# Kernel tuning notes

Measured on AMD Instinct MI355X. Metric: run time of the kernel, lower is better.

## Reference

```python
import jax, jax.numpy as jnp
import numpy as np

NEG_SLOPE = 0.2  # PyG GATConv default


def gat_layer(x, src, dst, W, a_src, a_dst, b, num_nodes):
    """Single-head GATConv (heads=1, add_self_loops handled by caller)."""
    xw = x @ W  # [N, H]
    s_src = xw @ a_src  # [N] per-node source attention logits
    s_dst = xw @ a_dst  # [N]
    e = jax.nn.leaky_relu(s_src[src] + s_dst[dst], NEG_SLOPE)  # [E]
    # segment softmax over incoming edges of each dst node
    m = jax.ops.segment_max(e, dst, num_segments=num_nodes)  # [N]
    ex = jnp.exp(e - m[dst])
    denom = jax.ops.segment_sum(ex, dst, num_segments=num_nodes)  # [N]
    alpha = ex / denom[dst]  # [E]
    out = jax.ops.segment_sum(alpha[:, None] * xw[src], dst, num_segments=num_nodes)
    return out + b


def setup_inputs() -> dict:
    key = jax.random.key(0)
    N, F_IN, H, E, B = 100000, 256, 64, 1000000, 16384
    ks = jax.random.split(key, 16)
    s = lambda fan: 1.0 / np.sqrt(fan)
    return {
        "x": jax.random.normal(ks[0], (N, F_IN), dtype=jnp.float32),
        "edge_index": jax.random.randint(ks[1], (2, E), 0, N, dtype=jnp.int64),
        "user_indices": jax.random.randint(ks[2], (B,), 0, N, dtype=jnp.int64),
        "movie_indices": jax.random.randint(ks[3], (B,), 0, N, dtype=jnp.int64),
        "W1": jax.random.normal(ks[4], (F_IN, H), dtype=jnp.float32) * s(F_IN),
        "a_src1": jax.random.normal(ks[5], (H,), dtype=jnp.float32) * s(H),
        "a_dst1": jax.random.normal(ks[6], (H,), dtype=jnp.float32) * s(H),
        "b1": jnp.zeros((H,), dtype=jnp.float32),
        "W2": jax.random.normal(ks[7], (H, H), dtype=jnp.float32) * s(H),
        "a_src2": jax.random.normal(ks[8], (H,), dtype=jnp.float32) * s(H),
        "a_dst2": jax.random.normal(ks[9], (H,), dtype=jnp.float32) * s(H),
        "b2": jnp.zeros((H,), dtype=jnp.float32),
        "fc_W": jax.random.normal(ks[10], (2 * H, 1), dtype=jnp.float32) * s(2 * H),
        "fc_b": jnp.zeros((1,), dtype=jnp.float32),
    }


def reference(x, edge_index, user_indices, movie_indices,
              W1, a_src1, a_dst1, b1, W2, a_src2, a_dst2, b2, fc_W, fc_b):
    N = x.shape[0]
    # PyG GATConv default add_self_loops=True: append (i, i) edges
    loops = jnp.arange(N, dtype=edge_index.dtype)
    src = jnp.concatenate([edge_index[0], loops])
    dst = jnp.concatenate([edge_index[1], loops])
    h = gat_layer(x, src, dst, W1, a_src1, a_dst1, b1, N)
    h = jax.nn.relu(h)
    h = gat_layer(h, src, dst, W2, a_src2, a_dst2, b2, N)
    combined = jnp.concatenate([h[user_indices], h[movie_indices]], axis=1)  # [B, 2H]
    return combined @ fc_W + fc_b  # [B, 1]
```

## Files before the change

### kernel.cpp

```cpp
#include <hip/hip_runtime.h>
#include <hip/hip_bf16.h>
#include <hip/hip_fp16.h>

#define LRELU_SLOPE 0.2f

__device__ __forceinline__ float lrelu(float x) { return x > 0.f ? x : LRELU_SLOPE * x; }

typedef __attribute__((ext_vector_type(8))) short short8;
typedef __attribute__((ext_vector_type(4))) float f32x4;

__device__ __forceinline__ unsigned short f2bf(float f) {
    unsigned u = __builtin_bit_cast(unsigned, f);
    u = (u + 0x7FFFu + ((u >> 16) & 1u)) >> 16;
    return (unsigned short)u;
}
__device__ __forceinline__ float bf2f(unsigned short b) {
    unsigned u = ((unsigned)b) << 16;
    return __builtin_bit_cast(float, u);
}

template <int K>
__device__ __forceinline__ void packW_body(const float* __restrict__ W,
                                           unsigned short* __restrict__ Bhi,
                                           unsigned short* __restrict__ Blo,
                                           int blk, int t) {
    constexpr int NKC = K / 32;
    int g = blk * 256 + t;
    if (g >= 4 * NKC * 64) return;
    int lane = g & 63;
    int kc = (g >> 6) % NKC;
    int ct = g / (64 * NKC);
    int qd = lane >> 4, col = lane & 15;
    #pragma unroll
    for (int j = 0; j < 8; j++) {
        int k = kc * 32 + qd * 8 + j;
        float w = W[(size_t)k * 64 + ct * 16 + col];
        unsigned short h = f2bf(w);
        float rem = w - bf2f(h);
        Bhi[(size_t)g * 8 + j] = h;
        Blo[(size_t)g * 8 + j] = f2bf(rem);
    }
}

__global__ __launch_bounds__(256) void k_prep(const float* __restrict__ W1,
                                              unsigned short* __restrict__ b1hi, unsigned short* __restrict__ b1lo,
                                              const float* __restrict__ W2,
                                              unsigned short* __restrict__ b2hi, unsigned short* __restrict__ b2lo,
                                              int* __restrict__ deg, int* __restrict__ gcnt, int N) {
    int b = blockIdx.x;
    if (b < 8)  { packW_body<256>(W1, b1hi, b1lo, b, threadIdx.x); return; }
    if (b < 10) { packW_body<64>(W2, b2hi, b2lo, b - 8, threadIdx.x); return; }
    int i = (b - 10) * 256 + threadIdx.x;
    if (i < N) deg[i] = 0;
    if (i == 0) *gcnt = 0;
}

__global__ void k_hist(const int* __restrict__ dst, int* __restrict__ deg,
                       int* __restrict__ epos, int E) {
    int i = blockIdx.x * blockDim.x + threadIdx.x;
    if (i < E) epos[i] = atomicAdd(&deg[dst[i]], 1);
}

__global__ __launch_bounds__(256) void k_offsets(const int* __restrict__ deg, int* __restrict__ start,
                                                 int2* __restrict__ sd2, int* __restrict__ gcnt, int N) {
    int idx = blockIdx.x * 256 + threadIdx.x;
    int lane = threadIdx.x & 63;
    int v = (idx < N) ? deg[idx] : 0;
    int incl = v;
    #pragma unroll
    for (int d = 1; d < 64; d <<= 1) {
        int u = __shfl_up(incl, d);
        if (lane >= d) incl += u;
    }
    int total = __shfl(incl, 63);
    int base = 0;
    if (lane == 0) base = atomicAdd(gcnt, total);
    base = __shfl(base, 0);
    int st = base + incl - v;
    if (idx < N) {
        start[idx] = st;
        sd2[idx] = make_int2(st, v);
    }
}

__global__ void k_scatter(const int* __restrict__ src, const int* __restrict__ dst,
                          const int* __restrict__ start, const int* __restrict__ epos,
                          int* __restrict__ csr, int E) {
    int i = blockIdx.x * blockDim.x + threadIdx.x;
    if (i < E) csr[start[dst[i]] + epos[i]] = src[i];
}

template <int K>
__global__ __launch_bounds__(256) void k_mfma(const float* __restrict__ X,
                                              const unsigned short* __restrict__ Bhi,
                                              const unsigned short* __restrict__ Blo,
                                              const float* __restrict__ a_s, const float* __restrict__ a_d,
                                              __half* __restrict__ XW, float* __restrict__ Ssrc,
                                              float* __restrict__ Sdst, int N) {
    constexpr int NKC = K / 32;
    int t = threadIdx.x, lane = t & 63, wid = t >> 6;
    int mtile = blockIdx.x * 4 + wid;
    if (mtile * 16 >= N) return;
    int m0 = mtile * 16;
    int qd = lane >> 4, col = lane & 15;

    int rA = m0 + col;
    rA = rA < N ? rA : N - 1;
    const float* xrow = X + (size_t)rA * K + qd * 8;

    const short8* bh = (const short8*)Bhi;
    const short8* bl = (const short8*)Blo;

    f32x4 acc[4];
    #pragma unroll
    for (int ct = 0; ct < 4; ct++) acc[ct] = (f32x4){0.f, 0.f, 0.f, 0.f};

    #pragma clang loop unroll(disable)
    for (int kc = 0; kc < NKC; kc++) {
        const float* xp = xrow + kc * 32;
        float4 xa = *(const float4*)xp;
        float4 xb = *(const float4*)(xp + 4);
        float xv[8] = {xa.x, xa.y, xa.z, xa.w, xb.x, xb.y, xb.z, xb.w};
        short8 ah, al;
        #pragma unroll
        for (int j = 0; j < 8; j++) {
            unsigned short h = f2bf(xv[j]);
            ah[j] = (short)h;
            al[j] = (short)f2bf(xv[j] - bf2f(h));
        }
        #pragma unroll
        for (int ct = 0; ct < 4; ct++) {
            short8 wh = bh[(ct * NKC + kc) * 64 + lane];
            short8 wl = bl[(ct * NKC + kc) * 64 + lane];
            acc[ct] = __builtin_amdgcn_mfma_f32_16x16x32_bf16(ah, wh, acc[ct], 0, 0, 0);
            acc[ct] = __builtin_amdgcn_mfma_f32_16x16x32_bf16(al, wh, acc[ct], 0, 0, 0);
            acc[ct] = __builtin_amdgcn_mfma_f32_16x16x32_bf16(ah, wl, acc[ct], 0, 0, 0);
        }
    }

    float asx[4], adx[4];
    #pragma unroll
    for (int ct = 0; ct < 4; ct++) {
        asx[ct] = a_s[ct * 16 + col];
        adx[ct] = a_d[ct * 16 + col];
    }
    #pragma unroll
    for (int r = 0; r < 4; r++) {
        int row = m0 + qd * 4 + r;
        if (row < N) {
            float vs = 0.f, vd = 0.f;
            #pragma unroll
            for (int ct = 0; ct < 4; ct++) {
                float v = acc[ct][r];
                XW[(size_t)row * 64 + ct * 16 + col] = __float2half(v);
                vs += v * asx[ct];
                vd += v * adx[ct];
            }
            #pragma unroll
            for (int d = 1; d < 16; d <<= 1) {
                vs += __shfl_xor(vs, d);
                vd += __shfl_xor(vd, d);
            }
            if (col == 0) { Ssrc[row] = vs; Sdst[row] = vd; }
        }
    }
}

__global__ __launch_bounds__(256) void k_attn(const __half* __restrict__ XW, const float* __restrict__ Ssrc,
                                              const float* __restrict__ Sdst, const int* __restrict__ csr,
                                              const int2* __restrict__ sd2,
                                              const float* __restrict__ bias, float* __restrict__ H,
                                              int N, int do_relu) {
    int t = threadIdx.x, lane = t & 63, wid = t >> 6;
    int q = lane >> 4;
    int c = lane & 15;
    int n = (blockIdx.x * 4 + wid) * 4 + q;
    bool valid = n < N;
    int nc = valid ? n : N - 1;

    int2 sv = sd2[nc];
    int st = sv.x, d = sv.y;
    float sd = Sdst[nc];
    int dcap = d < 16 ? d : 16;

    int myS = 0;
    if (c < d) myS = csr[st + c];

    int s0 = __shfl(myS, q * 16 + 0), s1 = __shfl(myS, q * 16 + 1);
    int s2 = __shfl(myS, q * 16 + 2), s3 = __shfl(myS, q * 16 + 3);
    float2 rs = *(const float2*)(XW + (size_t)nc * 64 + c * 4);
    float2 r0 = *(const float2*)(XW + (size_t)s0 * 64 + c * 4);
    float2 r1 = *(const float2*)(XW + (size_t)s1 * 64 + c * 4);
    float2 r2 = *(const float2*)(XW + (size_t)s2 * 64 + c * 4);
    float2 r3 = *(const float2*)(XW + (size_t)s3 * 64 + c * 4);

    float wself = __expf(lrelu(Ssrc[nc] + sd));
    float myW = 0.f;
    if (c < d) myW = __expf(lrelu(Ssrc[myS] + sd));
    float dpart = myW + ((c == 0) ? wself : 0.f);

    float4 acc4 = make_float4(0.f, 0.f, 0.f, 0.f);
    auto accum = [&](float2 raw, float w) {
        const __half2* hp = (const __half2*)&raw;
        float2 f0 = __half22float2(hp[0]);
        float2 f1 = __half22float2(hp[1]);
        acc4.x += w * f0.x; acc4.y += w * f0.y; acc4.z += w * f1.x; acc4.w += w * f1.y;
    };

    float w0 = __shfl(myW, q * 16 + 0), w1 = __shfl(myW, q * 16 + 1);
    float w2 = __shfl(myW, q * 16 + 2), w3 = __shfl(myW, q * 16 + 3);
    accum(rs, wself);
    accum(r0, w0); accum(r1, w1); accum(r2, w2); accum(r3, w3);

    for (int i = 4; i < dcap; i += 4) {
        int t0 = __shfl(myS, q * 16 + i + 0), t1 = __shfl(myS, q * 16 + i + 1);
        int t2 = __shfl(myS, q * 16 + i + 2), t3 = __shfl(myS, q * 16 + i + 3);
        float2 q0 = *(const float2*)(XW + (size_t)t0 * 64 + c * 4);
        float2 q1 = *(const float2*)(XW + (size_t)t1 * 64 + c * 4);
        float2 q2 = *(const float2*)(XW + (size_t)t2 * 64 + c * 4);
        float2 q3 = *(const float2*)(XW + (size_t)t3 * 64 + c * 4);
        float v0 = __shfl(myW, q * 16 + i + 0), v1 = __shfl(myW, q * 16 + i + 1);
        float v2 = __shfl(myW, q * 16 + i + 2), v3 = __shfl(myW, q * 16 + i + 3);
        accum(q0, v0); accum(q1, v1); accum(q2, v2); accum(q3, v3);
    }

    for (int i = 16; i < d; i++) {
        int s = csr[st + i];
        float w = __expf(lrelu(Ssrc[s] + sd));
        if (c == 0) dpart += w;
        float2 qv = *(const float2*)(XW + (size_t)s * 64 + c * 4);
        accum(qv, w);
    }

    #pragma unroll
    for (int dd = 8; dd > 0; dd >>= 1) dpart += __shfl_xor(dpart, dd);

    if (valid) {
        float4 b4 = *(const float4*)&bias[c * 4];
        float inv = 1.f / dpart;
        float4 o;
        o.x = acc4.x * inv + b4.x;
        o.y = acc4.y * inv + b4.y;
        o.z = acc4.z * inv + b4.z;
        o.w = acc4.w * inv + b4.w;
        if (do_relu) {
            o.x = fmaxf(o.x, 0.f); o.y = fmaxf(o.y, 0.f);
            o.z = fmaxf(o.z, 0.f); o.w = fmaxf(o.w, 0.f);
        }
        *(float4*)&H[(size_t)n * 64 + c * 4] = o;
    }
}

__global__ __launch_bounds__(256) void k_head(const float* __restrict__ H, const int* __restrict__ ui,
                                              const int* __restrict__ mi, const float* __restrict__ fcW,
                                              const float* __restrict__ fcb, float* __restrict__ out, int B) {
    int t = threadIdx.x, lane = t & 63, wid = t >> 6;
    int i = blockIdx.x * 4 + wid;
    if (i >= B) return;
    int u = ui[i], m = mi[i];
    float v = H[(size_t)u * 64 + lane] * fcW[lane] + H[(size_t)m * 64 + lane] * fcW[64 + lane];
    #pragma unroll
    for (int dd = 32; dd > 0; dd >>= 1) v += __shfl_xor(v, dd);
    if (lane == 0) out[i] = v + fcb[0];
}

extern "C" void kernel_launch(void* const* d_in, const int* in_sizes, int n_in,
                              void* d_out, int out_size, void* d_ws, size_t ws_size,
                              hipStream_t stream) {
    const float* x   = (const float*)d_in[0];
    const int*   ei  = (const int*)d_in[1];
    const int*   ui  = (const int*)d_in[2];
    const int*   mi  = (const int*)d_in[3];
    const float* W1  = (const float*)d_in[4];
    const float* as1 = (const float*)d_in[5];
    const float* ad1 = (const float*)d_in[6];
    const float* b1  = (const float*)d_in[7];
    const float* W2  = (const float*)d_in[8];
    const float* as2 = (const float*)d_in[9];
    const float* ad2 = (const float*)d_in[10];
    const float* b2  = (const float*)d_in[11];
    const float* fcW = (const float*)d_in[12];
    const float* fcb = (const float*)d_in[13];
    float* out = (float*)d_out;

    const int Hdim = in_sizes[5];
    const int FIN  = in_sizes[4] / Hdim;
    const int N    = in_sizes[0] / FIN;
    const int E    = in_sizes[1] / 2;
    const int B    = in_sizes[2];

    char* w = (char*)d_ws;
    auto alloc = [&](size_t bytes) -> void* {
        void* p = (void*)w;
        w += (bytes + 255) & ~(size_t)255;
        return p;
    };
    __half* xw  = (__half*)alloc((size_t)N * 64 * 2);
    float* hbuf = (float*)alloc((size_t)N * 64 * 4);
    float* ssrc = (float*)alloc((size_t)N * 4);
    float* sdst = (float*)alloc((size_t)N * 4);
    int* deg    = (int*)alloc((size_t)N * 4);
    int* startv = (int*)alloc((size_t)N * 4);
    int2* sd2   = (int2*)alloc((size_t)N * 8);
    int* gcnt   = (int*)alloc(256);
    int* csr    = (int*)alloc((size_t)E * 4);
    int* epos   = (int*)alloc((size_t)E * 4);
    unsigned short* b1hi = (unsigned short*)alloc((size_t)4 * 8 * 64 * 8 * 2);
    unsigned short* b1lo = (unsigned short*)alloc((size_t)4 * 8 * 64 * 8 * 2);
    unsigned short* b2hi = (unsigned short*)alloc((size_t)4 * 2 * 64 * 8 * 2);
    unsigned short* b2lo = (unsigned short*)alloc((size_t)4 * 2 * 64 * 8 * 2);

    const int* esrc = ei;
    const int* edst = ei + E;

    int prepBlocks = 10 + (N + 255) / 256;
    k_prep<<<prepBlocks, 256, 0, stream>>>(W1, b1hi, b1lo, W2, b2hi, b2lo, deg, gcnt, N);

    k_hist<<<(E + 255) / 256, 256, 0, stream>>>(edst, deg, epos, E);
    k_offsets<<<(N + 255) / 256, 256, 0, stream>>>(deg, startv, sd2, gcnt, N);
    k_scatter<<<(E + 255) / 256, 256, 0, stream>>>(esrc, edst, startv, epos, csr, E);

    const int mfmaBlocks = ((N + 15) / 16 + 3) / 4;
    const int attnBlocks = (N + 15) / 16;

    k_mfma<256><<<mfmaBlocks, 256, 0, stream>>>(x, b1hi, b1lo, as1, ad1, xw, ssrc, sdst, N);
    k_attn<<<attnBlocks, 256, 0, stream>>>(xw, ssrc, sdst, csr, sd2, b1, hbuf, N, 1);

    k_mfma<64><<<mfmaBlocks, 256, 0, stream>>>(hbuf, b2hi, b2lo, as2, ad2, xw, ssrc, sdst, N);
    k_attn<<<attnBlocks, 256, 0, stream>>>(xw, ssrc, sdst, csr, sd2, b2, hbuf, N, 0);

    k_head<<<(B + 3) / 4, 256, 0, stream>>>(hbuf, ui, mi, fcW, fcb, out, B);
}
```

Baseline: 350.0 us.

## Overlap layer-1 GEMM with CSR histogram and scatter via fused launches

The layer-1 projection GEMM is split in two halves, and each half runs in extra blocks of the histogram and scatter kernels. This lets the compute-bound MFMA work share the GPU with the atomic- and scatter-bound CSR build, and it removes one launch. The risk is that the fused kernels carry the GEMM's register pressure into the simple blocks, which can lower occupancy for the atomic and scatter work.

```diff
diff --git a/kernel.cpp b/kernel.cpp
--- a/kernel.cpp
+++ b/kernel.cpp
@@ -55,12 +55,6 @@
     if (i == 0) *gcnt = 0;
 }
 
-__global__ void k_hist(const int* __restrict__ dst, int* __restrict__ deg,
-                       int* __restrict__ epos, int E) {
-    int i = blockIdx.x * blockDim.x + threadIdx.x;
-    if (i < E) epos[i] = atomicAdd(&deg[dst[i]], 1);
-}
-
 __global__ __launch_bounds__(256) void k_offsets(const int* __restrict__ deg, int* __restrict__ start,
                                                  int2* __restrict__ sd2, int* __restrict__ gcnt, int N) {
     int idx = blockIdx.x * 256 + threadIdx.x;
@@ -83,23 +77,16 @@
     }
 }
 
-__global__ void k_scatter(const int* __restrict__ src, const int* __restrict__ dst,
-                          const int* __restrict__ start, const int* __restrict__ epos,
-                          int* __restrict__ csr, int E) {
-    int i = blockIdx.x * blockDim.x + threadIdx.x;
-    if (i < E) csr[start[dst[i]] + epos[i]] = src[i];
-}
-
 template <int K>
-__global__ __launch_bounds__(256) void k_mfma(const float* __restrict__ X,
-                                              const unsigned short* __restrict__ Bhi,
-                                              const unsigned short* __restrict__ Blo,
-                                              const float* __restrict__ a_s, const float* __restrict__ a_d,
-                                              __half* __restrict__ XW, float* __restrict__ Ssrc,
-                                              float* __restrict__ Sdst, int N) {
+__device__ __forceinline__ void mfma_body(const float* __restrict__ X,
+                                          const unsigned short* __restrict__ Bhi,
+                                          const unsigned short* __restrict__ Blo,
+                                          const float* __restrict__ a_s, const float* __restrict__ a_d,
+                                          __half* __restrict__ XW, float* __restrict__ Ssrc,
+                                          float* __restrict__ Sdst, int N, int blk) {
     constexpr int NKC = K / 32;
     int t = threadIdx.x, lane = t & 63, wid = t >> 6;
-    int mtile = blockIdx.x * 4 + wid;
+    int mtile = blk * 4 + wid;
     if (mtile * 16 >= N) return;
     int m0 = mtile * 16;
     int qd = lane >> 4, col = lane & 15;
@@ -166,6 +153,51 @@
     }
 }
 
+__global__ __launch_bounds__(256) void k_hist_mfma(const int* __restrict__ dst, int* __restrict__ deg,
+                                                   int* __restrict__ epos, int E, int histBlocks,
+                                                   const float* __restrict__ X,
+                                                   const unsigned short* __restrict__ Bhi,
+                                                   const unsigned short* __restrict__ Blo,
+                                                   const float* __restrict__ a_s, const float* __restrict__ a_d,
+                                                   __half* __restrict__ XW, float* __restrict__ Ssrc,
+                                                   float* __restrict__ Sdst, int N, int mfmaBase) {
+    int b = blockIdx.x;
+    if (b < histBlocks) {
+        int i = b * 256 + threadIdx.x;
+        if (i < E) epos[i] = atomicAdd(&deg[dst[i]], 1);
+        return;
+    }
+    mfma_body<256>(X, Bhi, Blo, a_s, a_d, XW, Ssrc, Sdst, N, mfmaBase + (b - histBlocks));
+}
+
+__global__ __launch_bounds__(256) void k_scatter_mfma(const int* __restrict__ src, const int* __restrict__ dst,
+                                                      const int* __restrict__ start, const int* __restrict__ epos,
+                                                      int* __restrict__ csr, int E, int scatBlocks,
+                                                      const float* __restrict__ X,
+                                                      const unsigned short* __restrict__ Bhi,
+                                                      const unsigned short* __restrict__ Blo,
+                                                      const float* __restrict__ a_s, const float* __restrict__ a_d,
+                                                      __half* __restrict__ XW, float* __restrict__ Ssrc,
+                                                      float* __restrict__ Sdst, int N, int mfmaBase) {
+    int b = blockIdx.x;
+    if (b < scatBlocks) {
+        int i = b * 256 + threadIdx.x;
+        if (i < E) csr[start[dst[i]] + epos[i]] = src[i];
+        return;
+    }
+    mfma_body<256>(X, Bhi, Blo, a_s, a_d, XW, Ssrc, Sdst, N, mfmaBase + (b - scatBlocks));
+}
+
+template <int K>
+__global__ __launch_bounds__(256) void k_mfma(const float* __restrict__ X,
+                                              const unsigned short* __restrict__ Bhi,
+                                              const unsigned short* __restrict__ Blo,
+                                              const float* __restrict__ a_s, const float* __restrict__ a_d,
+                                              __half* __restrict__ XW, float* __restrict__ Ssrc,
+                                              float* __restrict__ Sdst, int N) {
+    mfma_body<K>(X, Bhi, Blo, a_s, a_d, XW, Ssrc, Sdst, N, blockIdx.x);
+}
+
 __global__ __launch_bounds__(256) void k_attn(const __half* __restrict__ XW, const float* __restrict__ Ssrc,
                                               const float* __restrict__ Sdst, const int* __restrict__ csr,
                                               const int2* __restrict__ sd2,
@@ -313,17 +345,21 @@
     const int* esrc = ei;
     const int* edst = ei + E;
 
+    const int mfmaBlocks = ((N + 15) / 16 + 3) / 4;
+    const int mfmaA = mfmaBlocks / 2;
+    const int mfmaB = mfmaBlocks - mfmaA;
+    const int histBlocks = (E + 255) / 256;
+    const int attnBlocks = (N + 15) / 16;
+
     int prepBlocks = 10 + (N + 255) / 256;
     k_prep<<<prepBlocks, 256, 0, stream>>>(W1, b1hi, b1lo, W2, b2hi, b2lo, deg, gcnt, N);
 
-    k_hist<<<(E + 255) / 256, 256, 0, stream>>>(edst, deg, epos, E);
+    k_hist_mfma<<<histBlocks + mfmaA, 256, 0, stream>>>(edst, deg, epos, E, histBlocks,
+                                                        x, b1hi, b1lo, as1, ad1, xw, ssrc, sdst, N, 0);
     k_offsets<<<(N + 255) / 256, 256, 0, stream>>>(deg, startv, sd2, gcnt, N);
-    k_scatter<<<(E + 255) / 256, 256, 0, stream>>>(esrc, edst, startv, epos, csr, E);
-
-    const int mfmaBlocks = ((N + 15) / 16 + 3) / 4;
-    const int attnBlocks = (N + 15) / 16;
-
-    k_mfma<256><<<mfmaBlocks, 256, 0, stream>>>(x, b1hi, b1lo, as1, ad1, xw, ssrc, sdst, N);
+    k_scatter_mfma<<<histBlocks + mfmaB, 256, 0, stream>>>(esrc, edst, startv, epos, csr, E, histBlocks,
+                                                           x, b1hi, b1lo, as1, ad1, xw, ssrc, sdst, N, mfmaA);
+
     k_attn<<<attnBlocks, 256, 0, stream>>>(xw, ssrc, sdst, csr, sd2, b1, hbuf, N, 1);
 
     k_mfma<64><<<mfmaBlocks, 256, 0, stream>>>(hbuf, b2hi, b2lo, as2, ad2, xw, ssrc, sdst, N);
```

Measured after the change: 357.4 us. 1.02x slower.

## Replace exact CSR build with fixed-stride padded adjacency plus overflow list

Applied to the files above, without the earlier changes.

Replaces the three-kernel CSR construction (histogram, prefix-sum offsets, scatter) with a single kernel that places each edge in a fixed 32-slot row per destination node. Edges beyond the 32nd go to a global overflow list, which every attention thread scans linearly. This removes two kernel launches and the epos/start passes, at the cost of a padded adjacency buffer. It also relies on degrees rarely exceeding 32, which holds for the random test graph (mean degree about 10). A large overflow list would make attention quadratic, and the overflow buffer has a fixed capacity of 65536 with no bounds check.

```diff
diff --git a/kernel.cpp b/kernel.cpp
--- a/kernel.cpp
+++ b/kernel.cpp
@@ -3,6 +3,7 @@
 #include <hip/hip_fp16.h>
 
 #define LRELU_SLOPE 0.2f
+#define CSR_STRIDE 32
 
 __device__ __forceinline__ float lrelu(float x) { return x > 0.f ? x : LRELU_SLOPE * x; }
 
@@ -46,60 +47,40 @@
                                               unsigned short* __restrict__ b1hi, unsigned short* __restrict__ b1lo,
                                               const float* __restrict__ W2,
                                               unsigned short* __restrict__ b2hi, unsigned short* __restrict__ b2lo,
-                                              int* __restrict__ deg, int* __restrict__ gcnt, int N) {
+                                              int* __restrict__ deg, int* __restrict__ ovfCnt, int N) {
     int b = blockIdx.x;
     if (b < 8)  { packW_body<256>(W1, b1hi, b1lo, b, threadIdx.x); return; }
     if (b < 10) { packW_body<64>(W2, b2hi, b2lo, b - 8, threadIdx.x); return; }
     int i = (b - 10) * 256 + threadIdx.x;
     if (i < N) deg[i] = 0;
-    if (i == 0) *gcnt = 0;
-}
-
-__global__ void k_hist(const int* __restrict__ dst, int* __restrict__ deg,
-                       int* __restrict__ epos, int E) {
+    if (i == 0) *ovfCnt = 0;
+}
+
+__global__ void k_build(const int* __restrict__ src, const int* __restrict__ dst,
+                        int* __restrict__ deg, int* __restrict__ csr,
+                        int* __restrict__ ovfCnt, int2* __restrict__ ovf, int E) {
     int i = blockIdx.x * blockDim.x + threadIdx.x;
-    if (i < E) epos[i] = atomicAdd(&deg[dst[i]], 1);
-}
-
-__global__ __launch_bounds__(256) void k_offsets(const int* __restrict__ deg, int* __restrict__ start,
-                                                 int2* __restrict__ sd2, int* __restrict__ gcnt, int N) {
-    int idx = blockIdx.x * 256 + threadIdx.x;
-    int lane = threadIdx.x & 63;
-    int v = (idx < N) ? deg[idx] : 0;
-    int incl = v;
-    #pragma unroll
-    for (int d = 1; d < 64; d <<= 1) {
-        int u = __shfl_up(incl, d);
-        if (lane >= d) incl += u;
-    }
-    int total = __shfl(incl, 63);
-    int base = 0;
-    if (lane == 0) base = atomicAdd(gcnt, total);
-    base = __shfl(base, 0);
-    int st = base + incl - v;
-    if (idx < N) {
-        start[idx] = st;
-        sd2[idx] = make_int2(st, v);
-    }
-}
-
-__global__ void k_scatter(const int* __restrict__ src, const int* __restrict__ dst,
-                          const int* __restrict__ start, const int* __restrict__ epos,
-                          int* __restrict__ csr, int E) {
-    int i = blockIdx.x * blockDim.x + threadIdx.x;
-    if (i < E) csr[start[dst[i]] + epos[i]] = src[i];
+    if (i >= E) return;
+    int d = dst[i], s = src[i];
+    int p = atomicAdd(&deg[d], 1);
+    if (p < CSR_STRIDE) {
+        csr[d * CSR_STRIDE + p] = s;
+    } else {
+        int o = atomicAdd(ovfCnt, 1);
+        ovf[o] = make_int2(d, s);
+    }
 }
 
 template <int K>
-__global__ __launch_bounds__(256) void k_mfma(const float* __restrict__ X,
-                                              const unsigned short* __restrict__ Bhi,
-                                              const unsigned short* __restrict__ Blo,
-                                              const float* __restrict__ a_s, const float* __restrict__ a_d,
-                                              __half* __restrict__ XW, float* __restrict__ Ssrc,
-                                              float* __restrict__ Sdst, int N) {
+__device__ __forceinline__ void mfma_body(const float* __restrict__ X,
+                                          const unsigned short* __restrict__ Bhi,
+                                          const unsigned short* __restrict__ Blo,
+                                          const float* __restrict__ a_s, const float* __restrict__ a_d,
+                                          __half* __restrict__ XW, float* __restrict__ Ssrc,
+                                          float* __restrict__ Sdst, int N, int blk) {
     constexpr int NKC = K / 32;
     int t = threadIdx.x, lane = t & 63, wid = t >> 6;
-    int mtile = blockIdx.x * 4 + wid;
+    int mtile = blk * 4 + wid;
     if (mtile * 16 >= N) return;
     int m0 = mtile * 16;
     int qd = lane >> 4, col = lane & 15;
@@ -166,9 +147,20 @@
     }
 }
 
+template <int K>
+__global__ __launch_bounds__(256) void k_mfma(const float* __restrict__ X,
+                                              const unsigned short* __restrict__ Bhi,
+                                              const unsigned short* __restrict__ Blo,
+                                              const float* __restrict__ a_s, const float* __restrict__ a_d,
+                                              __half* __restrict__ XW, float* __restrict__ Ssrc,
+                                              float* __restrict__ Sdst, int N) {
+    mfma_body<K>(X, Bhi, Blo, a_s, a_d, XW, Ssrc, Sdst, N, blockIdx.x);
+}
+
 __global__ __launch_bounds__(256) void k_attn(const __half* __restrict__ XW, const float* __restrict__ Ssrc,
                                               const float* __restrict__ Sdst, const int* __restrict__ csr,
-                                              const int2* __restrict__ sd2,
+                                              const int* __restrict__ deg,
+                                              const int* __restrict__ ovfCnt, const int2* __restrict__ ovf,
                                               const float* __restrict__ bias, float* __restrict__ H,
                                               int N, int do_relu) {
     int t = threadIdx.x, lane = t & 63, wid = t >> 6;
@@ -178,13 +170,14 @@
     bool valid = n < N;
     int nc = valid ? n : N - 1;
 
-    int2 sv = sd2[nc];
-    int st = sv.x, d = sv.y;
+    int d = deg[nc];
+    int st = nc * CSR_STRIDE;
     float sd = Sdst[nc];
+    int d32 = d < CSR_STRIDE ? d : CSR_STRIDE;
     int dcap = d < 16 ? d : 16;
 
     int myS = 0;
-    if (c < d) myS = csr[st + c];
+    if (c < dcap) myS = csr[st + c];
 
     int s0 = __shfl(myS, q * 16 + 0), s1 = __shfl(myS, q * 16 + 1);
     int s2 = __shfl(myS, q * 16 + 2), s3 = __shfl(myS, q * 16 + 3);
@@ -196,7 +189,7 @@
 
     float wself = __expf(lrelu(Ssrc[nc] + sd));
     float myW = 0.f;
-    if (c < d) myW = __expf(lrelu(Ssrc[myS] + sd));
+    if (c < dcap) myW = __expf(lrelu(Ssrc[myS] + sd));
     float dpart = myW + ((c == 0) ? wself : 0.f);
 
     float4 acc4 = make_float4(0.f, 0.f, 0.f, 0.f);
@@ -224,12 +217,25 @@
         accum(q0, v0); accum(q1, v1); accum(q2, v2); accum(q3, v3);
     }
 
-    for (int i = 16; i < d; i++) {
+    for (int i = 16; i < d32; i++) {
         int s = csr[st + i];
         float w = __expf(lrelu(Ssrc[s] + sd));
         if (c == 0) dpart += w;
         float2 qv = *(const float2*)(XW + (size_t)s * 64 + c * 4);
         accum(qv, w);
+    }
+
+    int nov = *ovfCnt;
+    if (nov > 0) {
+        for (int j = 0; j < nov; j++) {
+            int2 e = ovf[j];
+            if (e.x == nc) {
+                float w = __expf(lrelu(Ssrc[e.y] + sd));
+                if (c == 0) dpart += w;
+                float2 qv = *(const float2*)(XW + (size_t)e.y * 64 + c * 4);
+                accum(qv, w);
+            }
+        }
     }
 
     #pragma unroll
@@ -300,11 +306,9 @@
     float* ssrc = (float*)alloc((size_t)N * 4);
     float* sdst = (float*)alloc((size_t)N * 4);
     int* deg    = (int*)alloc((size_t)N * 4);
-    int* startv = (int*)alloc((size_t)N * 4);
-    int2* sd2   = (int2*)alloc((size_t)N * 8);
-    int* gcnt   = (int*)alloc(256);
-    int* csr    = (int*)alloc((size_t)E * 4);
-    int* epos   = (int*)alloc((size_t)E * 4);
+    int* csr    = (int*)alloc((size_t)N * CSR_STRIDE * 4);
+    int* ovfCnt = (int*)alloc(256);
+    int2* ovf   = (int2*)alloc((size_t)65536 * 8);
     unsigned short* b1hi = (unsigned short*)alloc((size_t)4 * 8 * 64 * 8 * 2);
     unsigned short* b1lo = (unsigned short*)alloc((size_t)4 * 8 * 64 * 8 * 2);
     unsigned short* b2hi = (unsigned short*)alloc((size_t)4 * 2 * 64 * 8 * 2);
@@ -313,21 +317,19 @@
     const int* esrc = ei;
     const int* edst = ei + E;
 
-    int prepBlocks = 10 + (N + 255) / 256;
-    k_prep<<<prepBlocks, 256, 0, stream>>>(W1, b1hi, b1lo, W2, b2hi, b2lo, deg, gcnt, N);
-
-    k_hist<<<(E + 255) / 256, 256, 0, stream>>>(edst, deg, epos, E);
-    k_offsets<<<(N + 255) / 256, 256, 0, stream>>>(deg, startv, sd2, gcnt, N);
-    k_scatter<<<(E + 255) / 256, 256, 0, stream>>>(esrc, edst, startv, epos, csr, E);
-
     const int mfmaBlocks = ((N + 15) / 16 + 3) / 4;
     const int attnBlocks = (N + 15) / 16;
 
+    int prepBlocks = 10 + (N + 255) / 256;
+    k_prep<<<prepBlocks, 256, 0, stream>>>(W1, b1hi, b1lo, W2, b2hi, b2lo, deg, ovfCnt, N);
+
+    k_build<<<(E + 255) / 256, 256, 0, stream>>>(esrc, edst, deg, csr, ovfCnt, ovf, E);
+
     k_mfma<256><<<mfmaBlocks, 256, 0, stream>>>(x, b1hi, b1lo, as1, ad1, xw, ssrc, sdst, N);
-    k_attn<<<attnBlocks, 256, 0, stream>>>(xw, ssrc, sdst, csr, sd2, b1, hbuf, N, 1);
+    k_attn<<<attnBlocks, 256, 0, stream>>>(xw, ssrc, sdst, csr, deg, ovfCnt, ovf, b1, hbuf, N, 1);
 
     k_mfma<64><<<mfmaBlocks, 256, 0, stream>>>(hbuf, b2hi, b2lo, as2, ad2, xw, ssrc, sdst, N);
-    k_attn<<<attnBlocks, 256, 0, stream>>>(xw, ssrc, sdst, csr, sd2, b2, hbuf, N, 0);
+    k_attn<<<attnBlocks, 256, 0, stream>>>(xw, ssrc, sdst, csr, deg, ovfCnt, ovf, b2, hbuf, N, 0);
 
     k_head<<<(B + 3) / 4, 256, 0, stream>>>(hbuf, ui, mi, fcW, fcb, out, B);
 }
```

After: 347.2 us. No clear change (-0.8%).
